# Kernel optimization log

Measured on AMD Instinct MI355X. Metric: run time of the kernel, lower is better.

Reference implementation:

```python
import jax, jax.numpy as jnp
import numpy as np

DOWNSAMPLE = 4
REG = 0.05
SINKHORN_ITERS = 50
LAMBDA_OT = 1.0
LAMBDA_TV = 1.0


def setup_inputs() -> dict:
    key = jax.random.key(0)
    k1, k2 = jax.random.split(key)
    pred = jax.random.uniform(k1, (16, 1, 256, 256), dtype=jnp.float32)
    gt = jax.random.uniform(k2, (16, 1, 256, 256), dtype=jnp.float32)
    return {"pred": pred, "gt": gt, "epoch": 5, "max_epoch": 10}


def _avg_pool(x, k):
    B, C, H, W = x.shape
    return x.reshape(B, C, H // k, k, W // k, k).mean(axis=(3, 5))


def _normalize(x, n):
    # relu then normalize to a distribution; fall back to uniform if sum==0
    x = jnp.maximum(x, 0.0)
    s = x.sum(axis=1, keepdims=True)  # [B,1]
    return jnp.where(s > 0, x / s, jnp.full_like(x, 1.0 / n))


def _curriculum_loss(pred, gt, epoch, max_epoch):
    B = pred.shape[0]
    # --- counting loss: L1 between total counts ---
    pc = pred.reshape(B, -1).sum(axis=1)
    gc = gt.reshape(B, -1).sum(axis=1)
    l_count = jnp.abs(pc - gc).mean()

    t = float(epoch) / float(max(1, max_epoch))
    ot_w = LAMBDA_OT * t
    tv_w = LAMBDA_TV * t

    # --- OT loss (batched Sinkhorn) ---
    pd = _avg_pool(pred, DOWNSAMPLE)
    gd = _avg_pool(gt, DOWNSAMPLE)
    h, w = pd.shape[2], pd.shape[3]
    n = h * w
    ys = jnp.arange(h, dtype=jnp.float32)
    xs = jnp.arange(w, dtype=jnp.float32)
    yy, xx = jnp.meshgrid(ys, xs, indexing="ij")
    yf = yy.reshape(-1)  # [n]
    xf = xx.reshape(-1)
    # squared euclidean cost matrix [n,n], built separably (no [n,n,2] temp)
    M = (yf[:, None] - yf[None, :]) ** 2 + (xf[:, None] - xf[None, :]) ** 2
    K = jnp.exp(-M / REG)  # [n,n]

    a = _normalize(pd.reshape(B, -1), n)  # [B,n]
    b = _normalize(gd.reshape(B, -1), n)

    def step(uv, _):
        u, v = uv
        u = a / (v @ K.T)  # K @ v per sample, batched
        v = b / (u @ K)    # K.T @ u per sample, batched
        return (u, v), None

    ones = jnp.ones((B, n), dtype=pred.dtype)
    (u, v), _ = jax.lax.scan(step, (ones, ones), None, length=SINKHORN_ITERS)
    # cost_b = sum_ij u_i K_ij v_j M_ij
    cost = jnp.einsum("bn,nm,bm->b", u, K * M, v)
    l_ot = cost.mean()

    # --- total variation loss ---
    dx = jnp.abs(pred[:, :, :, 1:] - pred[:, :, :, :-1]).mean()
    dy = jnp.abs(pred[:, :, 1:, :] - pred[:, :, :-1, :]).mean()
    l_tv = dx + dy

    return l_count + ot_w * l_ot + tv_w * l_tv


def reference(pred, gt, epoch, max_epoch):
    return _curriculum_loss(pred, gt, epoch, max_epoch)
```

## Files before the change

kernel.cpp:

```cpp
#include <hip/hip_runtime.h>
#include <math.h>


#define KW1 2.0611536224385578e-09f
#define MW2 8.4967085105831778e-18f
#define RP2 72
#define PDOFF 2048
#define GDOFF 67584

__device__ __forceinline__ float dpp_right(float x) {
  return __int_as_float(__builtin_amdgcn_update_dpp(
      0, __float_as_int(x), 0x101, 0xF, 0xF, true));
}
__device__ __forceinline__ float dpp_left(float x) {
  return __int_as_float(__builtin_amdgcn_update_dpp(
      0, __float_as_int(x), 0x111, 0xF, 0xF, true));
}
__device__ __forceinline__ float wshr1(float x) {
  return __int_as_float(__builtin_amdgcn_update_dpp(
      0, __float_as_int(x), 0x138, 0xF, 0xF, true));
}
__device__ __forceinline__ float wshl1(float x) {
  return __int_as_float(__builtin_amdgcn_update_dpp(
      0, __float_as_int(x), 0x130, 0xF, 0xF, true));
}

__device__ __forceinline__ float ad4(const float4 a, const float4 b) {
  return fabsf(a.x - b.x) + fabsf(a.y - b.y) + fabsf(a.z - b.z) + fabsf(a.w - b.w);
}
__device__ __forceinline__ float agent_ld(const float* p) {
  return __hip_atomic_load(p, __ATOMIC_RELAXED, __HIP_MEMORY_SCOPE_AGENT);
}

__global__ __launch_bounds__(256) void prep_kernel(
    const float* __restrict__ pred, const float* __restrict__ gt,
    float* __restrict__ ws, unsigned int* __restrict__ cnt) {
  __shared__ float rbuf[16];
  const int g = blockIdx.x;
  const int im = g >> 4, band = g & 15;
  const int t = threadIdx.x;
  if (g == 0 && t == 0) *cnt = 0u;
  const int ppy = t >> 6, ppx = t & 63;
  const float* pb = pred + im * 65536;
  const float* gb = gt + im * 65536;
  const int sr0 = band * 16 + ppy * 4;
  const int c0 = ppx * 4;

  float4 q[4];
  float ps = 0.f, gs = 0.f, sx = 0.f, sy = 0.f;
#pragma unroll
  for (int r = 0; r < 4; ++r) {
    q[r] = *(const float4*)(pb + (sr0 + r) * 256 + c0);
    const float4 e = *(const float4*)(gb + (sr0 + r) * 256 + c0);
    ps += (q[r].x + q[r].y) + (q[r].z + q[r].w);
    gs += (e.x + e.y) + (e.z + e.w);
    sx += fabsf(q[r].y - q[r].x) + fabsf(q[r].z - q[r].y) + fabsf(q[r].w - q[r].z);
    const float nf = __shfl_down(q[r].x, 1);
    if (ppx < 63) sx += fabsf(nf - q[r].w);
  }
  sy += ad4(q[1], q[0]) + ad4(q[2], q[1]) + ad4(q[3], q[2]);
  if (sr0 + 4 < 256) {
    const float4 qn = *(const float4*)(pb + (sr0 + 4) * 256 + c0);
    sy += ad4(qn, q[3]);
  }
  const int prow = band * 4 + ppy;
  ws[PDOFF + im * 4096 + prow * 64 + ppx] = fmaxf(ps * 0.0625f, 0.f);
  ws[GDOFF + im * 4096 + prow * 64 + ppx] = fmaxf(gs * 0.0625f, 0.f);

  float r0 = ps, r1 = gs, r2 = sx, r3 = sy;
#pragma unroll
  for (int o = 32; o > 0; o >>= 1) {
    r0 += __shfl_down(r0, o); r1 += __shfl_down(r1, o);
    r2 += __shfl_down(r2, o); r3 += __shfl_down(r3, o);
  }
  if ((t & 63) == 0) {
    const int w = t >> 6;
    rbuf[w * 4 + 0] = r0; rbuf[w * 4 + 1] = r1;
    rbuf[w * 4 + 2] = r2; rbuf[w * 4 + 3] = r3;
  }
  __syncthreads();
  if (t == 0) {
    float a0 = 0, a1 = 0, a2 = 0, a3 = 0;
    for (int w = 0; w < 4; ++w) {
      a0 += rbuf[w * 4]; a1 += rbuf[w * 4 + 1];
      a2 += rbuf[w * 4 + 2]; a3 += rbuf[w * 4 + 3];
    }
    ws[g] = a0; ws[256 + g] = a1; ws[512 + g] = a2; ws[768 + g] = a3;
  }
}

__global__ __launch_bounds__(1024) void sink_kernel(
    float* __restrict__ ws, const int* __restrict__ epoch,
    const int* __restrict__ max_epoch, float* __restrict__ out,
    unsigned int* __restrict__ cnt) {
  __shared__ float SuL[18 * 64], SuR[18 * 64], SvL[18 * 64], SvR[18 * 64];
  __shared__ float rbuf[40];
  __shared__ int lastflag;

  const int b = blockIdx.x;
  const int t = threadIdx.x;
  const int w = t >> 6;
  const int l = t & 63;

  for (int i = t; i < 18 * 64; i += 1024) {
    SuL[i] = 0.f; SuR[i] = 0.f; SvL[i] = 0.f; SvR[i] = 0.f;
  }

  float av[4], bv[4];
  const float4 qa = *(const float4*)&ws[PDOFF + b * 4096 + l * 64 + 4 * w];
  const float4 qb = *(const float4*)&ws[GDOFF + b * 4096 + l * 64 + 4 * w];
  av[0] = qa.x; av[1] = qa.y; av[2] = qa.z; av[3] = qa.w;
  bv[0] = qb.x; bv[1] = qb.y; bv[2] = qb.z; bv[3] = qb.w;
  float spd = (qa.x + qa.y) + (qa.z + qa.w);
  float sgd = (qb.x + qb.y) + (qb.z + qb.w);
#pragma unroll
  for (int o = 32; o > 0; o >>= 1) {
    spd += __shfl_down(spd, o); sgd += __shfl_down(sgd, o);
  }
  if (l == 0) { rbuf[w * 2] = spd; rbuf[w * 2 + 1] = sgd; }
  __syncthreads();
  float Sp = 0.f, Sg = 0.f;
#pragma unroll
  for (int k = 0; k < 16; ++k) { Sp += rbuf[2 * k]; Sg += rbuf[2 * k + 1]; }

#pragma unroll
  for (int j = 0; j < 4; ++j) {
    av[j] = (Sp > 0.f) ? (av[j] / Sp) : (1.f / 4096.f);
    bv[j] = (Sg > 0.f) ? (bv[j] / Sg) : (1.f / 4096.f);
  }

  const int rdL = w * 64 + l;
  const int rdR = (w + 2) * 64 + l;
  const int wr  = (w + 1) * 64 + l;

  float uu[4], vv[4] = {1.f, 1.f, 1.f, 1.f}, hh[4];
  SvL[wr] = 1.f; SvR[wr] = 1.f;
  __syncthreads();

#pragma unroll 1
  for (int it = 0; it < 50; ++it) {
    {
      const float xl = SvR[rdL];
      const float xr = SvL[rdR];
      hh[0] = fmaf(KW1, xl + vv[1], vv[0]);
      hh[1] = fmaf(KW1, vv[0] + vv[2], vv[1]);
      hh[2] = fmaf(KW1, vv[1] + vv[3], vv[2]);
      hh[3] = fmaf(KW1, vv[2] + xr, vv[3]);
#pragma unroll
      for (int c = 0; c < 4; ++c) {
        const float d = fmaf(KW1, wshr1(hh[c]) + wshl1(hh[c]), hh[c]);
        uu[c] = av[c] * __builtin_amdgcn_rcpf(d);
      }
      SuL[wr] = uu[0]; SuR[wr] = uu[3];
    }
    __syncthreads();
    {
      const float xl = SuR[rdL];
      const float xr = SuL[rdR];
      hh[0] = fmaf(KW1, xl + uu[1], uu[0]);
      hh[1] = fmaf(KW1, uu[0] + uu[2], uu[1]);
      hh[2] = fmaf(KW1, uu[1] + uu[3], uu[2]);
      hh[3] = fmaf(KW1, uu[2] + xr, uu[3]);
#pragma unroll
      for (int c = 0; c < 4; ++c) {
        const float d = fmaf(KW1, wshr1(hh[c]) + wshl1(hh[c]), hh[c]);
        vv[c] = bv[c] * __builtin_amdgcn_rcpf(d);
      }
      SvL[wr] = vv[0]; SvR[wr] = vv[3];
    }
    __syncthreads();
  }

  float c = 0.f;
  {
    const float xl = SvR[rdL];
    const float xr = SvL[rdR];
#pragma unroll
    for (int cc = 0; cc < 4; ++cc) {
      const float vl = (cc == 0) ? xl : vv[cc - 1];
      const float vr = (cc == 3) ? xr : vv[cc + 1];
      const float s = vl + vr;
      const float e = (wshr1(vv[cc]) + wshl1(vv[cc])) + s;
      const float d = wshr1(s) + wshl1(s);
      c += uu[cc] * fmaf(MW2, d, KW1 * e);
    }
  }
#pragma unroll
  for (int o = 32; o > 0; o >>= 1) c += __shfl_down(c, o);
  if (l == 0) rbuf[w] = c;
  __syncthreads();
  if (t == 0) {
    float s = 0.f;
    for (int k = 0; k < 16; ++k) s += rbuf[k];
    ws[1024 + b] = s;
    __threadfence();
    const unsigned int old = atomicAdd(cnt, 1u);
    lastflag = (old == 15u) ? 1 : 0;
  }
  __syncthreads();

  if (lastflag) {
    __threadfence();
    float myPc = 0.f, myGc = 0.f, myTx = 0.f, myTy = 0.f;
    if (t < 256) {
      myPc = agent_ld(&ws[t]);
      myGc = agent_ld(&ws[256 + t]);
      myTx = agent_ld(&ws[512 + t]);
      myTy = agent_ld(&ws[768 + t]);
    }
#pragma unroll
    for (int o = 8; o > 0; o >>= 1) {
      myPc += __shfl_down(myPc, o, 16);
      myGc += __shfl_down(myGc, o, 16);
    }
    float d = ((t & 15) == 0) ? fabsf(myPc - myGc) : 0.f;
    float ct = (t < 16) ? agent_ld(&ws[1024 + t]) : 0.f;
#pragma unroll
    for (int o = 32; o > 0; o >>= 1) {
      d += __shfl_down(d, o); ct += __shfl_down(ct, o);
      myTx += __shfl_down(myTx, o); myTy += __shfl_down(myTy, o);
    }
    if ((t & 63) == 0 && t < 256) {
      const int ww = t >> 6;
      rbuf[16 + ww * 4] = d; rbuf[16 + ww * 4 + 1] = ct;
      rbuf[16 + ww * 4 + 2] = myTx; rbuf[16 + ww * 4 + 3] = myTy;
    }
    __syncthreads();
    if (t == 0) {
      float lc = 0, lot = 0, tvx = 0, tvy = 0;
      for (int ww = 0; ww < 4; ++ww) {
        lc += rbuf[16 + ww * 4]; lot += rbuf[16 + ww * 4 + 1];
        tvx += rbuf[16 + ww * 4 + 2]; tvy += rbuf[16 + ww * 4 + 3];
      }
      int me = max_epoch[0]; if (me < 1) me = 1;
      const float tt = (float)epoch[0] / (float)me;
      const float ltv = tvx / (16.f * 256.f * 255.f) + tvy / (16.f * 255.f * 256.f);
      out[0] = lc * (1.f / 16.f) + tt * (lot * (1.f / 16.f)) + tt * ltv;
    }
  }
}

__device__ __forceinline__ void hrow4(const float f[4], float h[4]) {
  const float l = dpp_left(f[3]);
  const float r = dpp_right(f[0]);
  h[0] = fmaf(KW1, l + f[1], f[0]);
  h[1] = fmaf(KW1, f[0] + f[2], f[1]);
  h[2] = fmaf(KW1, f[1] + f[3], f[2]);
  h[3] = fmaf(KW1, f[2] + r, f[3]);
}
__device__ __forceinline__ void phase_core(
    const float prev[4][4], float ph[4][4],
    const float cf0[4], const float cf3[4],
    float2 mA, float4 mB, float2 mC, float2 pA, float4 pB, float2 pC,
    float* __restrict__ RT_wr, float* __restrict__ RB_wr, int wb,
    float out0[4], float out3[4]) {
  hrow4(prev[0], ph[0]); hrow4(prev[1], ph[1]);
  hrow4(prev[2], ph[2]); hrow4(prev[3], ph[3]);
  float hm[4], hp[4];
  hm[0] = fmaf(KW1, mA.y + mB.y, mB.x);
  hm[1] = fmaf(KW1, mB.x + mB.z, mB.y);
  hm[2] = fmaf(KW1, mB.y + mB.w, mB.z);
  hm[3] = fmaf(KW1, mB.z + mC.x, mB.w);
  hp[0] = fmaf(KW1, pA.y + pB.y, pB.x);
  hp[1] = fmaf(KW1, pB.x + pB.z, pB.y);
  hp[2] = fmaf(KW1, pB.y + pB.w, pB.z);
  hp[3] = fmaf(KW1, pB.z + pC.x, pB.w);
#pragma unroll
  for (int j = 0; j < 4; ++j)
    out0[j] = cf0[j] * __builtin_amdgcn_rcpf(fmaf(KW1, hm[j] + ph[1][j], ph[0][j]));
#pragma unroll
  for (int j = 0; j < 4; ++j)
    out3[j] = cf3[j] * __builtin_amdgcn_rcpf(fmaf(KW1, ph[2][j] + hp[j], ph[3][j]));
  *(float4*)&RT_wr[wb] = make_float4(out0[0], out0[1], out0[2], out0[3]);
  *(float4*)&RB_wr[wb] = make_float4(out3[0], out3[1], out3[2], out3[3]);
}

__global__ __launch_bounds__(256) void fused_fallback(
    const float* __restrict__ pred, const float* __restrict__ gt,
    float* __restrict__ ws, const int* __restrict__ epoch,
    const int* __restrict__ max_epoch, float* __restrict__ out,
    unsigned int* __restrict__ cnt) {
  __shared__ float RTu[18 * RP2], RBu[18 * RP2];
  __shared__ float RTv[18 * RP2], RBv[18 * RP2];
  __shared__ float rbuf[24];

  const int b = blockIdx.x;
  const int t = threadIdx.x;
  const int tyg = t >> 4, tx = t & 15;
  const int y0 = tyg * 4, x0 = tx * 4;

  for (int i = t; i < 18 * RP2; i += 256) {
    RTu[i] = 0.f; RBu[i] = 0.f; RTv[i] = 0.f; RBv[i] = 0.f;
  }

  const float* pb = pred + b * 65536;
  const float* gb = gt + b * 65536;
  const int sr0 = 4 * y0, sc0 = 4 * x0;

  float pd[4][4], gd[4][4];
  float4 pr0, pr1, pr2, pr3;
  float spraw = 0.f, sgraw = 0.f, sx = 0.f, sy = 0.f;
#pragma unroll
  for (int i = 0; i < 4; ++i) {
    float a0 = 0.f, a1 = 0.f, a2 = 0.f, a3 = 0.f;
    float c0 = 0.f, c1 = 0.f, c2 = 0.f, c3 = 0.f;
#pragma unroll 1
    for (int rr = 0; rr < 4; ++rr) {
      const int r = i * 4 + rr;
      const float* prow = pb + (sr0 + r) * 256 + sc0;
      const float4 q0 = *(const float4*)(prow);
      const float4 q1 = *(const float4*)(prow + 4);
      const float4 q2 = *(const float4*)(prow + 8);
      const float4 q3 = *(const float4*)(prow + 12);
      const float s0 = (q0.x + q0.y) + (q0.z + q0.w);
      const float s1 = (q1.x + q1.y) + (q1.z + q1.w);
      const float s2 = (q2.x + q2.y) + (q2.z + q2.w);
      const float s3 = (q3.x + q3.y) + (q3.z + q3.w);
      a0 += s0; a1 += s1; a2 += s2; a3 += s3;
      spraw += (s0 + s1) + (s2 + s3);
      sx += fabsf(q0.y - q0.x) + fabsf(q0.z - q0.y) + fabsf(q0.w - q0.z)
          + fabsf(q1.x - q0.w)
          + fabsf(q1.y - q1.x) + fabsf(q1.z - q1.y) + fabsf(q1.w - q1.z)
          + fabsf(q2.x - q1.w)
          + fabsf(q2.y - q2.x) + fabsf(q2.z - q2.y) + fabsf(q2.w - q2.z)
          + fabsf(q3.x - q2.w)
          + fabsf(q3.y - q3.x) + fabsf(q3.z - q3.y) + fabsf(q3.w - q3.z);
      const float nf = dpp_right(q0.x);
      if (tx < 15) sx += fabsf(nf - q3.w);
      if (r > 0) sy += ad4(q0, pr0) + ad4(q1, pr1) + ad4(q2, pr2) + ad4(q3, pr3);
      pr0 = q0; pr1 = q1; pr2 = q2; pr3 = q3;
      const float* grow = gb + (sr0 + r) * 256 + sc0;
      const float4 g0 = *(const float4*)(grow);
      const float4 g1 = *(const float4*)(grow + 4);
      const float4 g2 = *(const float4*)(grow + 8);
      const float4 g3 = *(const float4*)(grow + 12);
      const float u0 = (g0.x + g0.y) + (g0.z + g0.w);
      const float u1 = (g1.x + g1.y) + (g1.z + g1.w);
      const float u2 = (g2.x + g2.y) + (g2.z + g2.w);
      const float u3 = (g3.x + g3.y) + (g3.z + g3.w);
      c0 += u0; c1 += u1; c2 += u2; c3 += u3;
      sgraw += (u0 + u1) + (u2 + u3);
    }
    pd[i][0] = a0; pd[i][1] = a1; pd[i][2] = a2; pd[i][3] = a3;
    gd[i][0] = c0; gd[i][1] = c1; gd[i][2] = c2; gd[i][3] = c3;
  }
  if (tyg < 15) {
    const float* prow = pb + (sr0 + 16) * 256 + sc0;
    sy += ad4(*(const float4*)(prow), pr0) + ad4(*(const float4*)(prow + 4), pr1)
        + ad4(*(const float4*)(prow + 8), pr2) + ad4(*(const float4*)(prow + 12), pr3);
  }

  float spd = 0.f, sgd = 0.f;
#pragma unroll
  for (int i = 0; i < 4; ++i)
#pragma unroll
    for (int j = 0; j < 4; ++j) {
      pd[i][j] = fmaxf(pd[i][j] * 0.0625f, 0.f); spd += pd[i][j];
      gd[i][j] = fmaxf(gd[i][j] * 0.0625f, 0.f); sgd += gd[i][j];
    }

  float r0 = spraw, r1 = sgraw, r2 = spd, r3 = sgd, r4 = sx, r5 = sy;
#pragma unroll
  for (int o = 32; o > 0; o >>= 1) {
    r0 += __shfl_down(r0, o); r1 += __shfl_down(r1, o);
    r2 += __shfl_down(r2, o); r3 += __shfl_down(r3, o);
    r4 += __shfl_down(r4, o); r5 += __shfl_down(r5, o);
  }
  if ((t & 63) == 0) {
    const int w = t >> 6;
    rbuf[w * 6 + 0] = r0; rbuf[w * 6 + 1] = r1; rbuf[w * 6 + 2] = r2;
    rbuf[w * 6 + 3] = r3; rbuf[w * 6 + 4] = r4; rbuf[w * 6 + 5] = r5;
  }
  __syncthreads();
  if (t == 0) {
    float a0 = 0, a1 = 0, a2 = 0, a3 = 0, a4 = 0, a5 = 0;
    for (int w = 0; w < 4; ++w) {
      a0 += rbuf[w * 6 + 0]; a1 += rbuf[w * 6 + 1]; a2 += rbuf[w * 6 + 2];
      a3 += rbuf[w * 6 + 3]; a4 += rbuf[w * 6 + 4]; a5 += rbuf[w * 6 + 5];
    }
    ws[b] = a0; ws[16 + b] = a1; ws[48 + b] = a4; ws[64 + b] = a5;
    rbuf[0] = a2; rbuf[1] = a3;
  }
  __syncthreads();
  const float Sp = rbuf[0], Sg = rbuf[1];

  float av[4][4], bv[4][4];
#pragma unroll
  for (int i = 0; i < 4; ++i)
#pragma unroll
    for (int j = 0; j < 4; ++j) {
      av[i][j] = (Sp > 0.f) ? (pd[i][j] / Sp) : (1.f / 4096.f);
      bv[i][j] = (Sg > 0.f) ? (gd[i][j] / Sg) : (1.f / 4096.f);
    }

  const int rbb = tyg * RP2 + x0 + 2;
  const int rtb = (tyg + 2) * RP2 + x0 + 2;
  const int wb  = (1 + tyg) * RP2 + 4 + x0;

  float uu[4][4], vv[4][4], uh[4][4], vh[4][4];
#pragma unroll
  for (int i = 0; i < 4; ++i)
#pragma unroll
    for (int j = 0; j < 4; ++j) vv[i][j] = 1.f;
  *(float4*)&RTv[wb] = make_float4(1.f, 1.f, 1.f, 1.f);
  *(float4*)&RBv[wb] = make_float4(1.f, 1.f, 1.f, 1.f);
  __syncthreads();

#pragma unroll 1
  for (int it = 0; it < 50; ++it) {
    {
      const float2 mA = *(const float2*)&RBv[rbb];
      const float4 mB = *(const float4*)&RBv[rbb + 2];
      const float2 mC = *(const float2*)&RBv[rbb + 6];
      const float2 pA = *(const float2*)&RTv[rtb];
      const float4 pB = *(const float4*)&RTv[rtb + 2];
      const float2 pC = *(const float2*)&RTv[rtb + 6];
      if (it != 0) {
#pragma unroll
        for (int j = 0; j < 4; ++j) {
          vv[1][j] = bv[1][j] * __builtin_amdgcn_rcpf(fmaf(KW1, uh[0][j] + uh[2][j], uh[1][j]));
          vv[2][j] = bv[2][j] * __builtin_amdgcn_rcpf(fmaf(KW1, uh[1][j] + uh[3][j], uh[2][j]));
        }
      }
      phase_core(vv, vh, av[0], av[3], mA, mB, mC, pA, pB, pC,
                 RTu, RBu, wb, uu[0], uu[3]);
    }
    __syncthreads();
    {
      const float2 mA = *(const float2*)&RBu[rbb];
      const float4 mB = *(const float4*)&RBu[rbb + 2];
      const float2 mC = *(const float2*)&RBu[rbb + 6];
      const float2 pA = *(const float2*)&RTu[rtb];
      const float4 pB = *(const float4*)&RTu[rtb + 2];
      const float2 pC = *(const float2*)&RTu[rtb + 6];
#pragma unroll
      for (int j = 0; j < 4; ++j) {
        uu[1][j] = av[1][j] * __builtin_amdgcn_rcpf(fmaf(KW1, vh[0][j] + vh[2][j], vh[1][j]));
        uu[2][j] = av[2][j] * __builtin_amdgcn_rcpf(fmaf(KW1, vh[1][j] + vh[3][j], vh[2][j]));
      }
      phase_core(uu, uh, bv[0], bv[3], mA, mB, mC, pA, pB, pC,
                 RTv, RBv, wb, vv[0], vv[3]);
    }
    __syncthreads();
  }
#pragma unroll
  for (int j = 0; j < 4; ++j) {
    vv[1][j] = bv[1][j] * __builtin_amdgcn_rcpf(fmaf(KW1, uh[0][j] + uh[2][j], uh[1][j]));
    vv[2][j] = bv[2][j] * __builtin_amdgcn_rcpf(fmaf(KW1, uh[1][j] + uh[3][j], uh[2][j]));
  }

  float c = 0.f;
  {
    const float2 mA = *(const float2*)&RBv[rbb];
    const float4 mB = *(const float4*)&RBv[rbb + 2];
    const float2 mC = *(const float2*)&RBv[rbb + 6];
    const float2 pA = *(const float2*)&RTv[rtb];
    const float4 pB = *(const float4*)&RTv[rtb + 2];
    const float2 pC = *(const float2*)&RTv[rtb + 6];
    float W[6][6];
    W[0][0] = mA.y; W[0][1] = mB.x; W[0][2] = mB.y;
    W[0][3] = mB.z; W[0][4] = mB.w; W[0][5] = mC.x;
    W[5][0] = pA.y; W[5][1] = pB.x; W[5][2] = pB.y;
    W[5][3] = pB.z; W[5][4] = pB.w; W[5][5] = pC.x;
#pragma unroll
    for (int i = 0; i < 4; ++i) {
      W[1 + i][0] = dpp_left(vv[i][3]);
      W[1 + i][5] = dpp_right(vv[i][0]);
#pragma unroll
      for (int j = 0; j < 4; ++j) W[1 + i][1 + j] = vv[i][j];
    }
#pragma unroll
    for (int i = 0; i < 4; ++i)
#pragma unroll
      for (int j = 0; j < 4; ++j) {
        const float e = (W[i][j + 1] + W[i + 2][j + 1])
                      + (W[i + 1][j] + W[i + 1][j + 2]);
        const float d = (W[i][j] + W[i][j + 2])
                      + (W[i + 2][j] + W[i + 2][j + 2]);
        c += uu[i][j] * fmaf(MW2, d, KW1 * e);
      }
  }
#pragma unroll
  for (int o = 32; o > 0; o >>= 1) c += __shfl_down(c, o);
  if ((t & 63) == 0) rbuf[t >> 6] = c;
  __syncthreads();
  if (t == 0) {
    ws[32 + b] = rbuf[0] + rbuf[1] + rbuf[2] + rbuf[3];
    __threadfence();
    const unsigned int old = atomicAdd(cnt, 1u);
    if (old == 15u) {
      __threadfence();
      float lc = 0.f, lot = 0.f, tvx = 0.f, tvy = 0.f;
      for (int k = 0; k < 16; ++k) {
        const float p = agent_ld(&ws[k]);
        const float g = agent_ld(&ws[16 + k]);
        const float ct = agent_ld(&ws[32 + k]);
        const float x = agent_ld(&ws[48 + k]);
        const float y = agent_ld(&ws[64 + k]);
        lc += fabsf(p - g); lot += ct; tvx += x; tvy += y;
      }
      int me = max_epoch[0]; if (me < 1) me = 1;
      const float tt = (float)epoch[0] / (float)me;
      const float ltv = tvx / (16.f * 256.f * 255.f) + tvy / (16.f * 255.f * 256.f);
      out[0] = lc * (1.f / 16.f) + tt * (lot * (1.f / 16.f)) + tt * ltv;
    }
  }
}

extern "C" void kernel_launch(void* const* d_in, const int* in_sizes, int n_in,
                              void* d_out, int out_size, void* d_ws, size_t ws_size,
                              hipStream_t stream) {
  const float* pred = (const float*)d_in[0];
  const float* gt   = (const float*)d_in[1];
  const int* epoch  = (const int*)d_in[2];
  const int* max_ep = (const int*)d_in[3];
  float* out = (float*)d_out;
  float* ws  = (float*)d_ws;

  if (ws_size >= 600000) {
    unsigned int* cnt = (unsigned int*)((char*)d_ws + 4160);
    prep_kernel<<<dim3(256), dim3(256), 0, stream>>>(pred, gt, ws, cnt);
    sink_kernel<<<dim3(16), dim3(1024), 0, stream>>>(ws, epoch, max_ep, out, cnt);
  } else {
    unsigned int* cnt = (unsigned int*)((char*)d_ws + 384);
    hipMemsetAsync(cnt, 0, 4, stream);
    fused_fallback<<<dim3(16), dim3(256), 0, stream>>>(pred, gt, ws, epoch,
                                                       max_ep, out, cnt);
  }
}
```

Before: 100.6 us.

## Fuse prep and Sinkhorn kernels into one launch with flag-based inter-block sync

Merges the pooling/TV prep kernel and the Sinkhorn kernel into a single 64-block launch. Each block does a quarter image of prep and publishes a magic-value flag; the first 16 blocks spin on those flags, run Sinkhorn, and block 0 waits on done flags to do the final reduction. This removes one kernel launch and the atomic counter, but relies on all 64 blocks being co-resident, and the magic flags are never reset between calls, so stale flags from a previous run could pass the wait early. Also packs the per-iteration FMAs into two-wide vectors.

```diff
diff --git a/kernel.cpp b/kernel.cpp
--- a/kernel.cpp
+++ b/kernel.cpp
@@ -7,6 +7,12 @@
 #define RP2 72
 #define PDOFF 2048
 #define GDOFF 67584
+#define PFLAG 1040
+#define DFLAG 1104
+#define MAGICP 0x5D1E9A37u
+#define MAGICD 0xA6F04C19u
+
+typedef float f32x2 __attribute__((ext_vector_type(2)));
 
 __device__ __forceinline__ float dpp_right(float x) {
   return __int_as_float(__builtin_amdgcn_update_dpp(
@@ -31,88 +37,118 @@
 __device__ __forceinline__ float agent_ld(const float* p) {
   return __hip_atomic_load(p, __ATOMIC_RELAXED, __HIP_MEMORY_SCOPE_AGENT);
 }
-
-__global__ __launch_bounds__(256) void prep_kernel(
+__device__ __forceinline__ unsigned int agent_ld_u32_acq(const unsigned int* p) {
+  return __hip_atomic_load(p, __ATOMIC_ACQUIRE, __HIP_MEMORY_SCOPE_AGENT);
+}
+__device__ __forceinline__ void agent_st_u32_rel(unsigned int* p, unsigned int v) {
+  __hip_atomic_store(p, v, __ATOMIC_RELEASE, __HIP_MEMORY_SCOPE_AGENT);
+}
+__device__ __forceinline__ f32x2 pk_fma2(f32x2 a, f32x2 b, f32x2 c) {
+#if __has_builtin(__builtin_elementwise_fma)
+  return __builtin_elementwise_fma(a, b, c);
+#else
+  f32x2 d; d.x = fmaf(a.x, b.x, c.x); d.y = fmaf(a.y, b.y, c.y); return d;
+#endif
+}
+
+__global__ __launch_bounds__(1024) void fused_kernel(
     const float* __restrict__ pred, const float* __restrict__ gt,
-    float* __restrict__ ws, unsigned int* __restrict__ cnt) {
-  __shared__ float rbuf[16];
+    float* __restrict__ ws, const int* __restrict__ epoch,
+    const int* __restrict__ max_epoch, float* __restrict__ out) {
+  __shared__ float SuL[18 * 64], SuR[18 * 64], SvL[18 * 64], SvR[18 * 64];
+  __shared__ float rbuf[64];
+
   const int g = blockIdx.x;
-  const int im = g >> 4, band = g & 15;
-  const int t = threadIdx.x;
-  if (g == 0 && t == 0) *cnt = 0u;
-  const int ppy = t >> 6, ppx = t & 63;
-  const float* pb = pred + im * 65536;
-  const float* gb = gt + im * 65536;
-  const int sr0 = band * 16 + ppy * 4;
-  const int c0 = ppx * 4;
-
-  float4 q[4];
-  float ps = 0.f, gs = 0.f, sx = 0.f, sy = 0.f;
-#pragma unroll
-  for (int r = 0; r < 4; ++r) {
-    q[r] = *(const float4*)(pb + (sr0 + r) * 256 + c0);
-    const float4 e = *(const float4*)(gb + (sr0 + r) * 256 + c0);
-    ps += (q[r].x + q[r].y) + (q[r].z + q[r].w);
-    gs += (e.x + e.y) + (e.z + e.w);
-    sx += fabsf(q[r].y - q[r].x) + fabsf(q[r].z - q[r].y) + fabsf(q[r].w - q[r].z);
-    const float nf = __shfl_down(q[r].x, 1);
-    if (ppx < 63) sx += fabsf(nf - q[r].w);
-  }
-  sy += ad4(q[1], q[0]) + ad4(q[2], q[1]) + ad4(q[3], q[2]);
-  if (sr0 + 4 < 256) {
-    const float4 qn = *(const float4*)(pb + (sr0 + 4) * 256 + c0);
-    sy += ad4(qn, q[3]);
-  }
-  const int prow = band * 4 + ppy;
-  ws[PDOFF + im * 4096 + prow * 64 + ppx] = fmaxf(ps * 0.0625f, 0.f);
-  ws[GDOFF + im * 4096 + prow * 64 + ppx] = fmaxf(gs * 0.0625f, 0.f);
-
-  float r0 = ps, r1 = gs, r2 = sx, r3 = sy;
-#pragma unroll
-  for (int o = 32; o > 0; o >>= 1) {
-    r0 += __shfl_down(r0, o); r1 += __shfl_down(r1, o);
-    r2 += __shfl_down(r2, o); r3 += __shfl_down(r3, o);
-  }
-  if ((t & 63) == 0) {
-    const int w = t >> 6;
-    rbuf[w * 4 + 0] = r0; rbuf[w * 4 + 1] = r1;
-    rbuf[w * 4 + 2] = r2; rbuf[w * 4 + 3] = r3;
-  }
-  __syncthreads();
-  if (t == 0) {
-    float a0 = 0, a1 = 0, a2 = 0, a3 = 0;
-    for (int w = 0; w < 4; ++w) {
-      a0 += rbuf[w * 4]; a1 += rbuf[w * 4 + 1];
-      a2 += rbuf[w * 4 + 2]; a3 += rbuf[w * 4 + 3];
-    }
-    ws[g] = a0; ws[256 + g] = a1; ws[512 + g] = a2; ws[768 + g] = a3;
-  }
-}
-
-__global__ __launch_bounds__(1024) void sink_kernel(
-    float* __restrict__ ws, const int* __restrict__ epoch,
-    const int* __restrict__ max_epoch, float* __restrict__ out,
-    unsigned int* __restrict__ cnt) {
-  __shared__ float SuL[18 * 64], SuR[18 * 64], SvL[18 * 64], SvR[18 * 64];
-  __shared__ float rbuf[40];
-  __shared__ int lastflag;
-
-  const int b = blockIdx.x;
+  const int im = g & 15;
+  const int qt = g >> 4;
   const int t = threadIdx.x;
   const int w = t >> 6;
   const int l = t & 63;
 
+  {
+    const int band = qt * 4 + (w >> 2);
+    const int ppy = w & 3;
+    const float* pb = pred + im * 65536;
+    const float* gb = gt + im * 65536;
+    const int sr0 = band * 16 + ppy * 4;
+    const int c0 = l * 4;
+
+    float4 q[4];
+    float ps = 0.f, gs = 0.f, sx = 0.f, sy = 0.f;
+#pragma unroll
+    for (int r = 0; r < 4; ++r) {
+      q[r] = *(const float4*)(pb + (sr0 + r) * 256 + c0);
+      const float4 e = *(const float4*)(gb + (sr0 + r) * 256 + c0);
+      ps += (q[r].x + q[r].y) + (q[r].z + q[r].w);
+      gs += (e.x + e.y) + (e.z + e.w);
+      sx += fabsf(q[r].y - q[r].x) + fabsf(q[r].z - q[r].y) + fabsf(q[r].w - q[r].z);
+      const float nf = __shfl_down(q[r].x, 1);
+      if (l < 63) sx += fabsf(nf - q[r].w);
+    }
+    sy += ad4(q[1], q[0]) + ad4(q[2], q[1]) + ad4(q[3], q[2]);
+    if (sr0 + 4 < 256) {
+      const float4 qn = *(const float4*)(pb + (sr0 + 4) * 256 + c0);
+      sy += ad4(qn, q[3]);
+    }
+    const int prow = band * 4 + ppy;
+    ws[PDOFF + im * 4096 + prow * 64 + l] = fmaxf(ps * 0.0625f, 0.f);
+    ws[GDOFF + im * 4096 + prow * 64 + l] = fmaxf(gs * 0.0625f, 0.f);
+
+    float r0 = ps, r1 = gs, r2 = sx, r3 = sy;
+#pragma unroll
+    for (int o = 32; o > 0; o >>= 1) {
+      r0 += __shfl_down(r0, o); r1 += __shfl_down(r1, o);
+      r2 += __shfl_down(r2, o); r3 += __shfl_down(r3, o);
+    }
+    if (l == 0) {
+      rbuf[w * 4 + 0] = r0; rbuf[w * 4 + 1] = r1;
+      rbuf[w * 4 + 2] = r2; rbuf[w * 4 + 3] = r3;
+    }
+    __syncthreads();
+    if (t < 4) {
+      float a0 = 0, a1 = 0, a2 = 0, a3 = 0;
+#pragma unroll
+      for (int k = 0; k < 4; ++k) {
+        const int i = (4 * t + k) * 4;
+        a0 += rbuf[i]; a1 += rbuf[i + 1]; a2 += rbuf[i + 2]; a3 += rbuf[i + 3];
+      }
+      const int gb_ = im * 16 + qt * 4 + t;
+      ws[gb_] = a0; ws[256 + gb_] = a1; ws[512 + gb_] = a2; ws[768 + gb_] = a3;
+    }
+    __syncthreads();
+    if (t == 0) {
+      __threadfence();
+      agent_st_u32_rel((unsigned int*)ws + PFLAG + g, MAGICP);
+    }
+  }
+  if (g >= 16) return;
+
+  if (t == 0) {
+    const unsigned int* fl = (const unsigned int*)ws + PFLAG;
+    for (;;) {
+      unsigned int ok = (agent_ld_u32_acq(fl + im) == MAGICP);
+      ok &= (agent_ld_u32_acq(fl + im + 16) == MAGICP);
+      ok &= (agent_ld_u32_acq(fl + im + 32) == MAGICP);
+      ok &= (agent_ld_u32_acq(fl + im + 48) == MAGICP);
+      if (ok) break;
+      __builtin_amdgcn_s_sleep(1);
+    }
+  }
+  __syncthreads();
+
   for (int i = t; i < 18 * 64; i += 1024) {
     SuL[i] = 0.f; SuR[i] = 0.f; SvL[i] = 0.f; SvR[i] = 0.f;
   }
 
-  float av[4], bv[4];
-  const float4 qa = *(const float4*)&ws[PDOFF + b * 4096 + l * 64 + 4 * w];
-  const float4 qb = *(const float4*)&ws[GDOFF + b * 4096 + l * 64 + 4 * w];
-  av[0] = qa.x; av[1] = qa.y; av[2] = qa.z; av[3] = qa.w;
-  bv[0] = qb.x; bv[1] = qb.y; bv[2] = qb.z; bv[3] = qb.w;
-  float spd = (qa.x + qa.y) + (qa.z + qa.w);
-  float sgd = (qb.x + qb.y) + (qb.z + qb.w);
+  float avv[4], bvv[4];
+  {
+    const float* pa = &ws[PDOFF + im * 4096 + l * 64 + 4 * w];
+    const float* pbv = &ws[GDOFF + im * 4096 + l * 64 + 4 * w];
+#pragma unroll
+    for (int j = 0; j < 4; ++j) { avv[j] = agent_ld(pa + j); bvv[j] = agent_ld(pbv + j); }
+  }
+  float spd = (avv[0] + avv[1]) + (avv[2] + avv[3]);
+  float sgd = (bvv[0] + bvv[1]) + (bvv[2] + bvv[3]);
 #pragma unroll
   for (int o = 32; o > 0; o >>= 1) {
     spd += __shfl_down(spd, o); sgd += __shfl_down(sgd, o);
@@ -122,18 +158,20 @@
   float Sp = 0.f, Sg = 0.f;
 #pragma unroll
   for (int k = 0; k < 16; ++k) { Sp += rbuf[2 * k]; Sg += rbuf[2 * k + 1]; }
-
 #pragma unroll
   for (int j = 0; j < 4; ++j) {
-    av[j] = (Sp > 0.f) ? (av[j] / Sp) : (1.f / 4096.f);
-    bv[j] = (Sg > 0.f) ? (bv[j] / Sg) : (1.f / 4096.f);
-  }
+    avv[j] = (Sp > 0.f) ? (avv[j] / Sp) : (1.f / 4096.f);
+    bvv[j] = (Sg > 0.f) ? (bvv[j] / Sg) : (1.f / 4096.f);
+  }
+  const f32x2 av01 = {avv[0], avv[1]}, av23 = {avv[2], avv[3]};
+  const f32x2 bv01 = {bvv[0], bvv[1]}, bv23 = {bvv[2], bvv[3]};
+  const f32x2 kw2 = {KW1, KW1};
 
   const int rdL = w * 64 + l;
   const int rdR = (w + 2) * 64 + l;
   const int wr  = (w + 1) * 64 + l;
 
-  float uu[4], vv[4] = {1.f, 1.f, 1.f, 1.f}, hh[4];
+  f32x2 uu01, uu23, vv01 = {1.f, 1.f}, vv23 = {1.f, 1.f};
   SvL[wr] = 1.f; SvR[wr] = 1.f;
   __syncthreads();
 
@@ -142,47 +180,59 @@
     {
       const float xl = SvR[rdL];
       const float xr = SvL[rdR];
-      hh[0] = fmaf(KW1, xl + vv[1], vv[0]);
-      hh[1] = fmaf(KW1, vv[0] + vv[2], vv[1]);
-      hh[2] = fmaf(KW1, vv[1] + vv[3], vv[2]);
-      hh[3] = fmaf(KW1, vv[2] + xr, vv[3]);
-#pragma unroll
-      for (int c = 0; c < 4; ++c) {
-        const float d = fmaf(KW1, wshr1(hh[c]) + wshl1(hh[c]), hh[c]);
-        uu[c] = av[c] * __builtin_amdgcn_rcpf(d);
-      }
-      SuL[wr] = uu[0]; SuR[wr] = uu[3];
+      f32x2 h01, h23;
+      h01.x = fmaf(KW1, xl + vv01.y, vv01.x);
+      h01.y = fmaf(KW1, vv01.x + vv23.x, vv01.y);
+      h23.x = fmaf(KW1, vv01.y + vv23.y, vv23.x);
+      h23.y = fmaf(KW1, vv23.x + xr, vv23.y);
+      const f32x2 up01 = {wshr1(h01.x), wshr1(h01.y)};
+      const f32x2 dn01 = {wshl1(h01.x), wshl1(h01.y)};
+      const f32x2 up23 = {wshr1(h23.x), wshr1(h23.y)};
+      const f32x2 dn23 = {wshl1(h23.x), wshl1(h23.y)};
+      const f32x2 d01 = pk_fma2(kw2, up01 + dn01, h01);
+      const f32x2 d23 = pk_fma2(kw2, up23 + dn23, h23);
+      const f32x2 r01 = {__builtin_amdgcn_rcpf(d01.x), __builtin_amdgcn_rcpf(d01.y)};
+      const f32x2 r23 = {__builtin_amdgcn_rcpf(d23.x), __builtin_amdgcn_rcpf(d23.y)};
+      uu01 = av01 * r01; uu23 = av23 * r23;
+      SuL[wr] = uu01.x; SuR[wr] = uu23.y;
     }
     __syncthreads();
     {
       const float xl = SuR[rdL];
       const float xr = SuL[rdR];
-      hh[0] = fmaf(KW1, xl + uu[1], uu[0]);
-      hh[1] = fmaf(KW1, uu[0] + uu[2], uu[1]);
-      hh[2] = fmaf(KW1, uu[1] + uu[3], uu[2]);
-      hh[3] = fmaf(KW1, uu[2] + xr, uu[3]);
-#pragma unroll
-      for (int c = 0; c < 4; ++c) {
-        const float d = fmaf(KW1, wshr1(hh[c]) + wshl1(hh[c]), hh[c]);
-        vv[c] = bv[c] * __builtin_amdgcn_rcpf(d);
-      }
-      SvL[wr] = vv[0]; SvR[wr] = vv[3];
+      f32x2 h01, h23;
+      h01.x = fmaf(KW1, xl + uu01.y, uu01.x);
+      h01.y = fmaf(KW1, uu01.x + uu23.x, uu01.y);
+      h23.x = fmaf(KW1, uu01.y + uu23.y, uu23.x);
+      h23.y = fmaf(KW1, uu23.x + xr, uu23.y);
+      const f32x2 up01 = {wshr1(h01.x), wshr1(h01.y)};
+      const f32x2 dn01 = {wshl1(h01.x), wshl1(h01.y)};
+      const f32x2 up23 = {wshr1(h23.x), wshr1(h23.y)};
+      const f32x2 dn23 = {wshl1(h23.x), wshl1(h23.y)};
+      const f32x2 d01 = pk_fma2(kw2, up01 + dn01, h01);
+      const f32x2 d23 = pk_fma2(kw2, up23 + dn23, h23);
+      const f32x2 r01 = {__builtin_amdgcn_rcpf(d01.x), __builtin_amdgcn_rcpf(d01.y)};
+      const f32x2 r23 = {__builtin_amdgcn_rcpf(d23.x), __builtin_amdgcn_rcpf(d23.y)};
+      vv01 = bv01 * r01; vv23 = bv23 * r23;
+      SvL[wr] = vv01.x; SvR[wr] = vv23.y;
     }
     __syncthreads();
   }
 
   float c = 0.f;
   {
+    const float vvv[4] = {vv01.x, vv01.y, vv23.x, vv23.y};
+    const float uuu[4] = {uu01.x, uu01.y, uu23.x, uu23.y};
     const float xl = SvR[rdL];
     const float xr = SvL[rdR];
 #pragma unroll
     for (int cc = 0; cc < 4; ++cc) {
-      const float vl = (cc == 0) ? xl : vv[cc - 1];
-      const float vr = (cc == 3) ? xr : vv[cc + 1];
+      const float vl = (cc == 0) ? xl : vvv[cc - 1];
+      const float vr = (cc == 3) ? xr : vvv[cc + 1];
       const float s = vl + vr;
-      const float e = (wshr1(vv[cc]) + wshl1(vv[cc])) + s;
+      const float e = (wshr1(vvv[cc]) + wshl1(vvv[cc])) + s;
       const float d = wshr1(s) + wshl1(s);
-      c += uu[cc] * fmaf(MW2, d, KW1 * e);
+      c += uuu[cc] * fmaf(MW2, d, KW1 * e);
     }
   }
 #pragma unroll
@@ -192,14 +242,23 @@
   if (t == 0) {
     float s = 0.f;
     for (int k = 0; k < 16; ++k) s += rbuf[k];
-    ws[1024 + b] = s;
+    ws[1024 + im] = s;
     __threadfence();
-    const unsigned int old = atomicAdd(cnt, 1u);
-    lastflag = (old == 15u) ? 1 : 0;
-  }
-  __syncthreads();
-
-  if (lastflag) {
+    agent_st_u32_rel((unsigned int*)ws + DFLAG + im, MAGICD);
+  }
+
+  if (g == 0) {
+    if (t == 0) {
+      const unsigned int* df = (const unsigned int*)ws + DFLAG;
+      for (;;) {
+        unsigned int ok = 1u;
+#pragma unroll
+        for (int k = 0; k < 16; ++k) ok &= (agent_ld_u32_acq(df + k) == MAGICD);
+        if (ok) break;
+        __builtin_amdgcn_s_sleep(1);
+      }
+    }
+    __syncthreads();
     __threadfence();
     float myPc = 0.f, myGc = 0.f, myTx = 0.f, myTy = 0.f;
     if (t < 256) {
@@ -518,9 +577,8 @@
   float* ws  = (float*)d_ws;
 
   if (ws_size >= 600000) {
-    unsigned int* cnt = (unsigned int*)((char*)d_ws + 4160);
-    prep_kernel<<<dim3(256), dim3(256), 0, stream>>>(pred, gt, ws, cnt);
-    sink_kernel<<<dim3(16), dim3(1024), 0, stream>>>(ws, epoch, max_ep, out, cnt);
+    fused_kernel<<<dim3(64), dim3(1024), 0, stream>>>(pred, gt, ws, epoch,
+                                                      max_ep, out);
   } else {
     unsigned int* cnt = (unsigned int*)((char*)d_ws + 384);
     hipMemsetAsync(cnt, 0, 4, stream);
```

Result: slower. 108.5 us (+7.8%).

## Exit Sinkhorn loop early once the scaling vector reaches an exact fixed point

Applied to the files above, without the earlier changes.

The Sinkhorn loop now runs as 25 double iterations. After each pair it compares the v vector bitwise with its value from the previous pair and votes across the block through shared flags. Once no lane changes it breaks out, because further iterations would reproduce the same state, so the result is unchanged. This saves the remaining iterations and their block barriers at the cost of a per-pair compare, a wave vote and one extra shared-flag read.

```diff
diff --git a/kernel.cpp b/kernel.cpp
--- a/kernel.cpp
+++ b/kernel.cpp
@@ -89,12 +89,43 @@
   }
 }
 
+#define UPHASE() do {                                                   \
+    const float xl = SvR[rdL];                                          \
+    const float xr = SvL[rdR];                                          \
+    hh[0] = fmaf(KW1, xl + vv[1], vv[0]);                               \
+    hh[1] = fmaf(KW1, vv[0] + vv[2], vv[1]);                            \
+    hh[2] = fmaf(KW1, vv[1] + vv[3], vv[2]);                            \
+    hh[3] = fmaf(KW1, vv[2] + xr, vv[3]);                               \
+    _Pragma("unroll")                                                   \
+    for (int c_ = 0; c_ < 4; ++c_) {                                    \
+      const float d_ = fmaf(KW1, wshr1(hh[c_]) + wshl1(hh[c_]), hh[c_]);\
+      uu[c_] = av[c_] * __builtin_amdgcn_rcpf(d_);                      \
+    }                                                                   \
+    SuL[wr] = uu[0]; SuR[wr] = uu[3];                                   \
+  } while (0)
+
+#define VPHASE() do {                                                   \
+    const float xl = SuR[rdL];                                          \
+    const float xr = SuL[rdR];                                          \
+    hh[0] = fmaf(KW1, xl + uu[1], uu[0]);                               \
+    hh[1] = fmaf(KW1, uu[0] + uu[2], uu[1]);                            \
+    hh[2] = fmaf(KW1, uu[1] + uu[3], uu[2]);                            \
+    hh[3] = fmaf(KW1, uu[2] + xr, uu[3]);                               \
+    _Pragma("unroll")                                                   \
+    for (int c_ = 0; c_ < 4; ++c_) {                                    \
+      const float d_ = fmaf(KW1, wshr1(hh[c_]) + wshl1(hh[c_]), hh[c_]);\
+      vv[c_] = bv[c_] * __builtin_amdgcn_rcpf(d_);                      \
+    }                                                                   \
+    SvL[wr] = vv[0]; SvR[wr] = vv[3];                                   \
+  } while (0)
+
 __global__ __launch_bounds__(1024) void sink_kernel(
     float* __restrict__ ws, const int* __restrict__ epoch,
     const int* __restrict__ max_epoch, float* __restrict__ out,
     unsigned int* __restrict__ cnt) {
   __shared__ float SuL[18 * 64], SuR[18 * 64], SvL[18 * 64], SvR[18 * 64];
   __shared__ float rbuf[40];
+  __shared__ int chgp[2];
   __shared__ int lastflag;
 
   const int b = blockIdx.x;
@@ -134,41 +165,34 @@
   const int wr  = (w + 1) * 64 + l;
 
   float uu[4], vv[4] = {1.f, 1.f, 1.f, 1.f}, hh[4];
+  float pvO[4] = {1.f, 1.f, 1.f, 1.f};
   SvL[wr] = 1.f; SvR[wr] = 1.f;
+  if (t == 0) { chgp[0] = 0; chgp[1] = 0; }
   __syncthreads();
 
 #pragma unroll 1
-  for (int it = 0; it < 50; ++it) {
+  for (int k = 0; k < 25; ++k) {
+    UPHASE();
+    __syncthreads();
+    VPHASE();
+    __syncthreads();
+    UPHASE();
+    __syncthreads();
+    VPHASE();
     {
-      const float xl = SvR[rdL];
-      const float xr = SvL[rdR];
-      hh[0] = fmaf(KW1, xl + vv[1], vv[0]);
-      hh[1] = fmaf(KW1, vv[0] + vv[2], vv[1]);
-      hh[2] = fmaf(KW1, vv[1] + vv[3], vv[2]);
-      hh[3] = fmaf(KW1, vv[2] + xr, vv[3]);
+      int same = 1;
 #pragma unroll
       for (int c = 0; c < 4; ++c) {
-        const float d = fmaf(KW1, wshr1(hh[c]) + wshl1(hh[c]), hh[c]);
-        uu[c] = av[c] * __builtin_amdgcn_rcpf(d);
-      }
-      SuL[wr] = uu[0]; SuR[wr] = uu[3];
-    }
-    __syncthreads();
-    {
-      const float xl = SuR[rdL];
-      const float xr = SuL[rdR];
-      hh[0] = fmaf(KW1, xl + uu[1], uu[0]);
-      hh[1] = fmaf(KW1, uu[0] + uu[2], uu[1]);
-      hh[2] = fmaf(KW1, uu[1] + uu[3], uu[2]);
-      hh[3] = fmaf(KW1, uu[2] + xr, uu[3]);
-#pragma unroll
-      for (int c = 0; c < 4; ++c) {
-        const float d = fmaf(KW1, wshr1(hh[c]) + wshl1(hh[c]), hh[c]);
-        vv[c] = bv[c] * __builtin_amdgcn_rcpf(d);
-      }
-      SvL[wr] = vv[0]; SvR[wr] = vv[3];
-    }
-    __syncthreads();
+        same &= (__float_as_int(vv[c]) == __float_as_int(pvO[c]));
+        pvO[c] = vv[c];
+      }
+      if (!__all(same)) {
+        if (l == 0) chgp[k & 1] = 1;
+      }
+      if (t == 0) chgp[(k + 1) & 1] = 0;
+    }
+    __syncthreads();
+    if (chgp[k & 1] == 0) break;
   }
 
   float c = 0.f;
```

Result: slower. 105.7 us (+5.0%).

## Use halo-redundant Sinkhorn half-steps to halve barriers per iteration

Applied to the files above, without the earlier changes.

Each wave now keeps a two-column halo of the marginals and scaling vectors, so it computes u for six columns and v for four using only neighbour data it already holds. Only v is exchanged through shared memory, with a double-buffered array, which leaves one __syncthreads per iteration instead of two. In exchange the u update does extra redundant work and each iteration writes and reads more LDS entries. The boundary handling zeroes out-of-field halo entries so edge results stay correct.

```diff
diff --git a/kernel.cpp b/kernel.cpp
--- a/kernel.cpp
+++ b/kernel.cpp
@@ -93,24 +93,22 @@
     float* __restrict__ ws, const int* __restrict__ epoch,
     const int* __restrict__ max_epoch, float* __restrict__ out,
     unsigned int* __restrict__ cnt) {
-  __shared__ float SuL[18 * 64], SuR[18 * 64], SvL[18 * 64], SvR[18 * 64];
+  __shared__ float SV[2 * 18 * 4 * 64];
   __shared__ float rbuf[40];
   __shared__ int lastflag;
+  const int PSTR = 18 * 4 * 64;
 
   const int b = blockIdx.x;
   const int t = threadIdx.x;
   const int w = t >> 6;
   const int l = t & 63;
 
-  for (int i = t; i < 18 * 64; i += 1024) {
-    SuL[i] = 0.f; SuR[i] = 0.f; SvL[i] = 0.f; SvR[i] = 0.f;
-  }
-
-  float av[4], bv[4];
-  const float4 qa = *(const float4*)&ws[PDOFF + b * 4096 + l * 64 + 4 * w];
-  const float4 qb = *(const float4*)&ws[GDOFF + b * 4096 + l * 64 + 4 * w];
-  av[0] = qa.x; av[1] = qa.y; av[2] = qa.z; av[3] = qa.w;
-  bv[0] = qb.x; bv[1] = qb.y; bv[2] = qb.z; bv[3] = qb.w;
+  for (int i = t; i < 2 * 18 * 4 * 64; i += 1024) SV[i] = 0.f;
+
+  const int baseA = PDOFF + b * 4096 + l * 64 + 4 * w;
+  const int baseB = GDOFF + b * 4096 + l * 64 + 4 * w;
+  const float4 qa = *(const float4*)&ws[baseA];
+  const float4 qb = *(const float4*)&ws[baseB];
   float spd = (qa.x + qa.y) + (qa.z + qa.w);
   float sgd = (qb.x + qb.y) + (qb.z + qb.w);
 #pragma unroll
@@ -123,66 +121,75 @@
 #pragma unroll
   for (int k = 0; k < 16; ++k) { Sp += rbuf[2 * k]; Sg += rbuf[2 * k + 1]; }
 
-#pragma unroll
-  for (int j = 0; j < 4; ++j) {
-    av[j] = (Sp > 0.f) ? (av[j] / Sp) : (1.f / 4096.f);
-    bv[j] = (Sg > 0.f) ? (bv[j] / Sg) : (1.f / 4096.f);
-  }
-
-  const int rdL = w * 64 + l;
-  const int rdR = (w + 2) * 64 + l;
-  const int wr  = (w + 1) * 64 + l;
-
-  float uu[4], vv[4] = {1.f, 1.f, 1.f, 1.f}, hh[4];
-  SvL[wr] = 1.f; SvR[wr] = 1.f;
-  __syncthreads();
+  float ae[8], be[8], ve[8], ue[8];
+  {
+    float rA[8], rB[8];
+    rA[2] = qa.x; rA[3] = qa.y; rA[4] = qa.z; rA[5] = qa.w;
+    rB[2] = qb.x; rB[3] = qb.y; rB[4] = qb.z; rB[5] = qb.w;
+    if (w > 0) {
+      const float2 ha = *(const float2*)&ws[baseA - 2];
+      const float2 hb = *(const float2*)&ws[baseB - 2];
+      rA[0] = ha.x; rA[1] = ha.y; rB[0] = hb.x; rB[1] = hb.y;
+    } else { rA[0] = 0.f; rA[1] = 0.f; rB[0] = 0.f; rB[1] = 0.f; }
+    if (w < 15) {
+      const float2 ha = *(const float2*)&ws[baseA + 4];
+      const float2 hb = *(const float2*)&ws[baseB + 4];
+      rA[6] = ha.x; rA[7] = ha.y; rB[6] = hb.x; rB[7] = hb.y;
+    } else { rA[6] = 0.f; rA[7] = 0.f; rB[6] = 0.f; rB[7] = 0.f; }
+#pragma unroll
+    for (int r = 0; r < 8; ++r) {
+      const bool infield = (w > 0 || r >= 2) && (w < 15 || r <= 5);
+      ae[r] = infield ? ((Sp > 0.f) ? (rA[r] / Sp) : (1.f / 4096.f)) : 0.f;
+      be[r] = infield ? ((Sg > 0.f) ? (rB[r] / Sg) : (1.f / 4096.f)) : 0.f;
+      ve[r] = infield ? 1.f : 0.f;
+      ue[r] = 0.f;
+    }
+  }
+
+  const int swr = ((w + 1) * 4) * 64 + l;
+  const int sL2 = (w * 4 + 2) * 64 + l;
+  const int sL3 = (w * 4 + 3) * 64 + l;
+  const int sR0 = ((w + 2) * 4 + 0) * 64 + l;
+  const int sR1 = ((w + 2) * 4 + 1) * 64 + l;
 
 #pragma unroll 1
   for (int it = 0; it < 50; ++it) {
-    {
-      const float xl = SvR[rdL];
-      const float xr = SvL[rdR];
-      hh[0] = fmaf(KW1, xl + vv[1], vv[0]);
-      hh[1] = fmaf(KW1, vv[0] + vv[2], vv[1]);
-      hh[2] = fmaf(KW1, vv[1] + vv[3], vv[2]);
-      hh[3] = fmaf(KW1, vv[2] + xr, vv[3]);
-#pragma unroll
-      for (int c = 0; c < 4; ++c) {
-        const float d = fmaf(KW1, wshr1(hh[c]) + wshl1(hh[c]), hh[c]);
-        uu[c] = av[c] * __builtin_amdgcn_rcpf(d);
-      }
-      SuL[wr] = uu[0]; SuR[wr] = uu[3];
-    }
+#pragma unroll
+    for (int r = 1; r <= 6; ++r) {
+      const float h = fmaf(KW1, ve[r - 1] + ve[r + 1], ve[r]);
+      const float d = fmaf(KW1, wshr1(h) + wshl1(h), h);
+      ue[r] = ae[r] * __builtin_amdgcn_rcpf(d);
+    }
+#pragma unroll
+    for (int r = 2; r <= 5; ++r) {
+      const float h = fmaf(KW1, ue[r - 1] + ue[r + 1], ue[r]);
+      const float d = fmaf(KW1, wshr1(h) + wshl1(h), h);
+      ve[r] = be[r] * __builtin_amdgcn_rcpf(d);
+    }
+    const int pb_ = (it & 1) * PSTR;
+    SV[pb_ + swr + 0 * 64] = ve[2];
+    SV[pb_ + swr + 1 * 64] = ve[3];
+    SV[pb_ + swr + 2 * 64] = ve[4];
+    SV[pb_ + swr + 3 * 64] = ve[5];
     __syncthreads();
-    {
-      const float xl = SuR[rdL];
-      const float xr = SuL[rdR];
-      hh[0] = fmaf(KW1, xl + uu[1], uu[0]);
-      hh[1] = fmaf(KW1, uu[0] + uu[2], uu[1]);
-      hh[2] = fmaf(KW1, uu[1] + uu[3], uu[2]);
-      hh[3] = fmaf(KW1, uu[2] + xr, uu[3]);
-#pragma unroll
-      for (int c = 0; c < 4; ++c) {
-        const float d = fmaf(KW1, wshr1(hh[c]) + wshl1(hh[c]), hh[c]);
-        vv[c] = bv[c] * __builtin_amdgcn_rcpf(d);
-      }
-      SvL[wr] = vv[0]; SvR[wr] = vv[3];
-    }
-    __syncthreads();
+    ve[0] = SV[pb_ + sL2]; ve[1] = SV[pb_ + sL3];
+    ve[6] = SV[pb_ + sR0]; ve[7] = SV[pb_ + sR1];
   }
 
   float c = 0.f;
   {
-    const float xl = SvR[rdL];
-    const float xr = SvL[rdR];
+    const float xl = ve[1];
+    const float xr = ve[6];
+    const float vvv[4] = {ve[2], ve[3], ve[4], ve[5]};
+    const float uuu[4] = {ue[2], ue[3], ue[4], ue[5]};
 #pragma unroll
     for (int cc = 0; cc < 4; ++cc) {
-      const float vl = (cc == 0) ? xl : vv[cc - 1];
-      const float vr = (cc == 3) ? xr : vv[cc + 1];
+      const float vl = (cc == 0) ? xl : vvv[cc - 1];
+      const float vr = (cc == 3) ? xr : vvv[cc + 1];
       const float s = vl + vr;
-      const float e = (wshr1(vv[cc]) + wshl1(vv[cc])) + s;
+      const float e = (wshr1(vvv[cc]) + wshl1(vvv[cc])) + s;
       const float d = wshr1(s) + wshl1(s);
-      c += uu[cc] * fmaf(MW2, d, KW1 * e);
+      c += uuu[cc] * fmaf(MW2, d, KW1 * e);
     }
   }
 #pragma unroll
```

After: 103.5 us. 1.03x slower.
